# Optimization experiments

Measured on AMD Instinct MI355X. Metric: run time of the kernel, lower is better.

Reference implementation:

```python
import jax, jax.numpy as jnp
import numpy as np

N = 4096
IN_DIM = 128
OUT_DIM = 64
LEAKY_SLOPE = 0.2


def setup_inputs() -> dict:
    key = jax.random.key(0)
    ks = jax.random.split(key, 8)
    H = jax.random.normal(ks[0], (N, IN_DIM), dtype=jnp.float32)
    # dense 0/1 adjacency per relation (int constants w.r.t. autodiff)
    A_buys = jax.random.randint(ks[1], (N, N), 0, 2, dtype=jnp.int32)
    A_views = jax.random.randint(ks[2], (N, N), 0, 2, dtype=jnp.int32)
    # xavier_uniform for W (stored [in, out]; Wh = H @ W == torch Linear with weight W.T)
    s_w = float(np.sqrt(6.0 / (IN_DIM + OUT_DIM)))
    W_buys = jax.random.uniform(ks[3], (IN_DIM, OUT_DIM), jnp.float32, -s_w, s_w)
    W_views = jax.random.uniform(ks[4], (IN_DIM, OUT_DIM), jnp.float32, -s_w, s_w)
    # xavier_uniform on a.view(1, 2*out_dim)
    s_a = float(np.sqrt(6.0 / (1 + 2 * OUT_DIM)))
    a_buys = jax.random.uniform(ks[5], (2 * OUT_DIM,), jnp.float32, -s_a, s_a)
    a_views = jax.random.uniform(ks[6], (2 * OUT_DIM,), jnp.float32, -s_a, s_a)
    bias = jnp.zeros((OUT_DIM,), dtype=jnp.float32)
    return {"H": H, "A_buys": A_buys, "A_views": A_views,
            "W_buys": W_buys, "W_views": W_views,
            "a_buys": a_buys, "a_views": a_views, "bias": bias}


def _relation(H, A, W, a):
    Wh = H @ W                                  # [N, OUT]
    # (cat(Wh_i, Wh_j) * a).sum(-1) == Wh_i @ a[:OUT] + Wh_j @ a[OUT:]
    s_i = Wh @ a[:OUT_DIM]                      # [N]
    s_j = Wh @ a[OUT_DIM:]                      # [N]
    e = jax.nn.leaky_relu(s_i[:, None] + s_j[None, :], LEAKY_SLOPE)  # [N, N]
    e = jnp.where(A == 0, -jnp.inf, e)
    alpha = jnp.nan_to_num(jax.nn.softmax(e, axis=1))                # isolated rows -> 0
    return alpha @ Wh                           # [N, OUT]


def reference(H, A_buys, A_views, W_buys, W_views, a_buys, a_views, bias):
    agg = _relation(H, A_buys, W_buys, a_buys) + _relation(H, A_views, W_views, a_views)
    return agg + bias
```

## Files before the change

### kernel.cpp

```cpp
#include <hip/hip_runtime.h>

#define NN 4096
#define IND 128
#define OUTD 64

typedef __attribute__((ext_vector_type(4))) float  floatx4;
typedef __attribute__((ext_vector_type(8))) __bf16 bf16x8;
typedef __attribute__((ext_vector_type(4))) int    intx4;

__device__ __forceinline__ unsigned short f2bf(float f) {
  unsigned int u = __float_as_uint(f);
  u += 0x7fffu + ((u >> 16) & 1u);
  return (unsigned short)(u >> 16);
}

__device__ __forceinline__ float wcalc(int a, float s) {
  float l = s > 0.f ? s : 0.2f * s;
  float e = __expf(l);
  return a != 0 ? e : 0.f;
}

__global__ __launch_bounds__(256) void gat_prep(
    const float* __restrict__ H,
    const float* __restrict__ W0, const float* __restrict__ W1,
    const float* __restrict__ av0, const float* __restrict__ av1,
    unsigned short* __restrict__ whT,
    float* __restrict__ sA,
    float* __restrict__ sB)
{
  const int rel = blockIdx.y;
  const float* __restrict__ W  = rel ? W1 : W0;
  const float* __restrict__ av = rel ? av1 : av0;
  const int i0 = blockIdx.x * 16;
  const int t = threadIdx.x;
  const int c = t & 63;
  const int wv = __builtin_amdgcn_readfirstlane(t >> 6);
  const float* __restrict__ hp = H + (size_t)(i0 + wv * 4) * IND;

  float acc0 = 0.f, acc1 = 0.f, acc2 = 0.f, acc3 = 0.f;
#pragma unroll 8
  for (int k = 0; k < IND; k += 4) {
    float4 h0 = *(const float4*)(hp + k);
    float4 h1 = *(const float4*)(hp + IND + k);
    float4 h2 = *(const float4*)(hp + 2 * IND + k);
    float4 h3 = *(const float4*)(hp + 3 * IND + k);
    float w0 = W[(k + 0) * OUTD + c];
    float w1 = W[(k + 1) * OUTD + c];
    float w2 = W[(k + 2) * OUTD + c];
    float w3 = W[(k + 3) * OUTD + c];
    acc0 += h0.x * w0 + h0.y * w1 + h0.z * w2 + h0.w * w3;
    acc1 += h1.x * w0 + h1.y * w1 + h1.z * w2 + h1.w * w3;
    acc2 += h2.x * w0 + h2.y * w1 + h2.z * w2 + h2.w * w3;
    acc3 += h3.x * w0 + h3.y * w1 + h3.z * w2 + h3.w * w3;
  }

  const float alo = av[c], ahi = av[OUTD + c];
  float pa0 = acc0 * alo, pa1 = acc1 * alo, pa2 = acc2 * alo, pa3 = acc3 * alo;
  float pb0 = acc0 * ahi, pb1 = acc1 * ahi, pb2 = acc2 * ahi, pb3 = acc3 * ahi;
#pragma unroll
  for (int off = 32; off >= 1; off >>= 1) {
    pa0 += __shfl_xor(pa0, off); pa1 += __shfl_xor(pa1, off);
    pa2 += __shfl_xor(pa2, off); pa3 += __shfl_xor(pa3, off);
    pb0 += __shfl_xor(pb0, off); pb1 += __shfl_xor(pb1, off);
    pb2 += __shfl_xor(pb2, off); pb3 += __shfl_xor(pb3, off);
  }
  const int ibase = i0 + wv * 4;
  if (c == 0) {
    float* sa = sA + rel * NN + ibase;
    float* sb = sB + rel * NN + ibase;
    sa[0] = pa0; sa[1] = pa1; sa[2] = pa2; sa[3] = pa3;
    sb[0] = pb0; sb[1] = pb1; sb[2] = pb2; sb[3] = pb3;
  }

  unsigned long long packed =
      (unsigned long long)f2bf(acc0)        | ((unsigned long long)f2bf(acc1) << 16) |
      ((unsigned long long)f2bf(acc2) << 32) | ((unsigned long long)f2bf(acc3) << 48);
  *(unsigned long long*)(whT + (size_t)(rel * OUTD + c) * NN + ibase) = packed;
}

__global__ __launch_bounds__(512) void gat_main(
    const int* __restrict__ A0, const int* __restrict__ A1,
    const unsigned short* __restrict__ whT,
    const float* __restrict__ sA, const float* __restrict__ sB,
    float* __restrict__ res)
{
  __shared__ float red[8][1024];
  __shared__ float dred[8][16];
  const int rel  = blockIdx.y;
  const int i0   = blockIdx.x * 16;
  const int t    = threadIdx.x;
  const int w    = t >> 6;
  const int lane = t & 63;
  const int m    = lane & 15;
  const int quad = lane >> 4;
  const int i    = i0 + m;
  const int* __restrict__ A = rel ? A1 : A0;
  const float si = sA[rel * NN + i];
  const float* __restrict__ sb = sB + rel * NN;
  const unsigned short* __restrict__ wh = whT + (size_t)rel * OUTD * NN;

  const int jbase = w * 512 + quad * 8;
  const int*            pA  = A  + (size_t)i * NN + jbase;
  const float*          psb = sb + jbase;
  const unsigned short* pb0 = wh + (size_t)(0 * 16 + m) * NN + jbase;
  const unsigned short* pb1 = wh + (size_t)(1 * 16 + m) * NN + jbase;
  const unsigned short* pb2 = wh + (size_t)(2 * 16 + m) * NN + jbase;
  const unsigned short* pb3 = wh + (size_t)(3 * 16 + m) * NN + jbase;

  floatx4 acc0 = {0.f, 0.f, 0.f, 0.f}, acc1 = acc0, acc2 = acc0, acc3 = acc0;
  float dsum = 0.f;

  for (int jt = 0; jt < 512; jt += 32) {
    intx4 a0 = __builtin_nontemporal_load((const intx4*)(pA + jt));
    intx4 a1 = __builtin_nontemporal_load((const intx4*)(pA + jt + 4));
    float4 s0 = *(const float4*)(psb + jt);
    float4 s1 = *(const float4*)(psb + jt + 4);
    bf16x8 b0 = *(const bf16x8*)(pb0 + jt);
    bf16x8 b1 = *(const bf16x8*)(pb1 + jt);
    bf16x8 b2 = *(const bf16x8*)(pb2 + jt);
    bf16x8 b3 = *(const bf16x8*)(pb3 + jt);

    float e0 = wcalc(a0[0], si + s0.x);
    float e1 = wcalc(a0[1], si + s0.y);
    float e2 = wcalc(a0[2], si + s0.z);
    float e3 = wcalc(a0[3], si + s0.w);
    float e4 = wcalc(a1[0], si + s1.x);
    float e5 = wcalc(a1[1], si + s1.y);
    float e6 = wcalc(a1[2], si + s1.z);
    float e7 = wcalc(a1[3], si + s1.w);
    dsum += ((e0 + e1) + (e2 + e3)) + ((e4 + e5) + (e6 + e7));

    bf16x8 af;
    af[0] = (__bf16)e0; af[1] = (__bf16)e1; af[2] = (__bf16)e2; af[3] = (__bf16)e3;
    af[4] = (__bf16)e4; af[5] = (__bf16)e5; af[6] = (__bf16)e6; af[7] = (__bf16)e7;

    acc0 = __builtin_amdgcn_mfma_f32_16x16x32_bf16(af, b0, acc0, 0, 0, 0);
    acc1 = __builtin_amdgcn_mfma_f32_16x16x32_bf16(af, b1, acc1, 0, 0, 0);
    acc2 = __builtin_amdgcn_mfma_f32_16x16x32_bf16(af, b2, acc2, 0, 0, 0);
    acc3 = __builtin_amdgcn_mfma_f32_16x16x32_bf16(af, b3, acc3, 0, 0, 0);
  }

  dsum += __shfl_xor(dsum, 16);
  dsum += __shfl_xor(dsum, 32);

#pragma unroll
  for (int r = 0; r < 4; r++) {
    const int row = quad * 4 + r;
    red[w][row * 64 + 0 * 16 + m] = acc0[r];
    red[w][row * 64 + 1 * 16 + m] = acc1[r];
    red[w][row * 64 + 2 * 16 + m] = acc2[r];
    red[w][row * 64 + 3 * 16 + m] = acc3[r];
  }
  if (lane < 16) dred[w][lane] = dsum;
  __syncthreads();

  const int c  = t & 63;
  const int r0 = t >> 6;
#pragma unroll
  for (int rr = r0; rr < 16; rr += 8) {
    float ns = 0.f, ds = 0.f;
#pragma unroll
    for (int ww = 0; ww < 8; ww++) { ns += red[ww][rr * 64 + c]; ds += dred[ww][rr]; }
    float rv = ds > 0.f ? ns / ds : 0.f;
    res[((size_t)rel * NN + i0 + rr) * OUTD + c] = rv;
  }
}

__global__ __launch_bounds__(256) void gat_combine(
    const float* __restrict__ res, const float* __restrict__ bias,
    float* __restrict__ out)
{
  const int idx = blockIdx.x * 256 + threadIdx.x;
  float4 r0 = ((const float4*)res)[idx];
  float4 r1 = ((const float4*)res)[idx + NN * OUTD / 4];
  float4 b  = ((const float4*)bias)[idx & 15];
  float4 o;
  o.x = r0.x + r1.x + b.x;
  o.y = r0.y + r1.y + b.y;
  o.z = r0.z + r1.z + b.z;
  o.w = r0.w + r1.w + b.w;
  ((float4*)out)[idx] = o;
}

extern "C" void kernel_launch(void* const* d_in, const int* in_sizes, int n_in,
                              void* d_out, int out_size, void* d_ws, size_t ws_size,
                              hipStream_t stream) {
  const float* H    = (const float*)d_in[0];
  const int*   A0   = (const int*)d_in[1];
  const int*   A1   = (const int*)d_in[2];
  const float* W0   = (const float*)d_in[3];
  const float* W1   = (const float*)d_in[4];
  const float* av0  = (const float*)d_in[5];
  const float* av1  = (const float*)d_in[6];
  const float* bias = (const float*)d_in[7];
  float* out = (float*)d_out;

  unsigned short* whT = (unsigned short*)d_ws;
  float* sA  = (float*)((char*)d_ws + 2u * OUTD * NN * 2u);
  float* sB  = sA + 2 * NN;
  float* res = sB + 2 * NN;

  gat_prep<<<dim3(NN / 16, 2), 256, 0, stream>>>(H, W0, W1, av0, av1, whT, sA, sB);
  gat_main<<<dim3(NN / 16, 2), 512, 0, stream>>>(A0, A1, whT, sA, sB, res);
  gat_combine<<<(NN * OUTD / 4) / 256, 256, 0, stream>>>(res, bias, out);
}
```

Baseline: 205.6 us.

## Split attention neighbor dimension across blocks with deferred softmax normalization

The main kernel now splits the j (neighbor) range into two halves across a third grid dimension, doubling the block count. Each block writes unnormalized numerator and denominator partials. The combine kernel sums the partials per relation and divides there. The goal is more parallelism to saturate memory bandwidth on the large adjacency reads, at the cost of extra partial writes and reads. The loop is also unrolled by 2.

```diff
diff --git a/kernel.cpp b/kernel.cpp
--- a/kernel.cpp
+++ b/kernel.cpp
@@ -3,6 +3,7 @@
 #define NN 4096
 #define IND 128
 #define OUTD 64
+#define NSPLIT 2
 
 typedef __attribute__((ext_vector_type(4))) float  floatx4;
 typedef __attribute__((ext_vector_type(8))) __bf16 bf16x8;
@@ -82,11 +83,13 @@
     const int* __restrict__ A0, const int* __restrict__ A1,
     const unsigned short* __restrict__ whT,
     const float* __restrict__ sA, const float* __restrict__ sB,
-    float* __restrict__ res)
+    float* __restrict__ numer,
+    float* __restrict__ denom)
 {
   __shared__ float red[8][1024];
   __shared__ float dred[8][16];
   const int rel  = blockIdx.y;
+  const int sp   = blockIdx.z;
   const int i0   = blockIdx.x * 16;
   const int t    = threadIdx.x;
   const int w    = t >> 6;
@@ -99,7 +102,7 @@
   const float* __restrict__ sb = sB + rel * NN;
   const unsigned short* __restrict__ wh = whT + (size_t)rel * OUTD * NN;
 
-  const int jbase = w * 512 + quad * 8;
+  const int jbase = sp * (NN / NSPLIT) + w * 256 + quad * 8;
   const int*            pA  = A  + (size_t)i * NN + jbase;
   const float*          psb = sb + jbase;
   const unsigned short* pb0 = wh + (size_t)(0 * 16 + m) * NN + jbase;
@@ -110,7 +113,8 @@
   floatx4 acc0 = {0.f, 0.f, 0.f, 0.f}, acc1 = acc0, acc2 = acc0, acc3 = acc0;
   float dsum = 0.f;
 
-  for (int jt = 0; jt < 512; jt += 32) {
+#pragma unroll 2
+  for (int jt = 0; jt < 256; jt += 32) {
     intx4 a0 = __builtin_nontemporal_load((const intx4*)(pA + jt));
     intx4 a1 = __builtin_nontemporal_load((const intx4*)(pA + jt + 4));
     float4 s0 = *(const float4*)(psb + jt);
@@ -156,29 +160,41 @@
 
   const int c  = t & 63;
   const int r0 = t >> 6;
+  const size_t base = ((size_t)rel * NSPLIT + sp) * NN;
 #pragma unroll
   for (int rr = r0; rr < 16; rr += 8) {
     float ns = 0.f, ds = 0.f;
 #pragma unroll
     for (int ww = 0; ww < 8; ww++) { ns += red[ww][rr * 64 + c]; ds += dred[ww][rr]; }
-    float rv = ds > 0.f ? ns / ds : 0.f;
-    res[((size_t)rel * NN + i0 + rr) * OUTD + c] = rv;
+    numer[(base + i0 + rr) * OUTD + c] = ns;
+    if (c == 0) denom[base + i0 + rr] = ds;
   }
 }
 
 __global__ __launch_bounds__(256) void gat_combine(
-    const float* __restrict__ res, const float* __restrict__ bias,
-    float* __restrict__ out)
+    const float* __restrict__ numer, const float* __restrict__ denom,
+    const float* __restrict__ bias, float* __restrict__ out)
 {
   const int idx = blockIdx.x * 256 + threadIdx.x;
-  float4 r0 = ((const float4*)res)[idx];
-  float4 r1 = ((const float4*)res)[idx + NN * OUTD / 4];
-  float4 b  = ((const float4*)bias)[idx & 15];
-  float4 o;
-  o.x = r0.x + r1.x + b.x;
-  o.y = r0.y + r1.y + b.y;
-  o.z = r0.z + r1.z + b.z;
-  o.w = r0.w + r1.w + b.w;
+  const int i  = idx >> 4;
+  const int c4 = idx & 15;
+  const float4* nv = (const float4*)numer;
+
+  float4 o = ((const float4*)bias)[c4];
+#pragma unroll
+  for (int rel = 0; rel < 2; rel++) {
+    float4 n = {0.f, 0.f, 0.f, 0.f};
+    float  d = 0.f;
+#pragma unroll
+    for (int s = 0; s < NSPLIT; s++) {
+      const size_t base = ((size_t)rel * NSPLIT + s) * NN + i;
+      float4 np = nv[base * 16 + c4];
+      n.x += np.x; n.y += np.y; n.z += np.z; n.w += np.w;
+      d += denom[base];
+    }
+    float inv = d > 0.f ? 1.f / d : 0.f;
+    o.x += n.x * inv; o.y += n.y * inv; o.z += n.z * inv; o.w += n.w * inv;
+  }
   ((float4*)out)[idx] = o;
 }
 
@@ -196,11 +212,12 @@
   float* out = (float*)d_out;
 
   unsigned short* whT = (unsigned short*)d_ws;
-  float* sA  = (float*)((char*)d_ws + 2u * OUTD * NN * 2u);
-  float* sB  = sA + 2 * NN;
-  float* res = sB + 2 * NN;
+  float* sA    = (float*)((char*)d_ws + 2u * OUTD * NN * 2u);
+  float* sB    = sA + 2 * NN;
+  float* numer = sB + 2 * NN;
+  float* denom = numer + (size_t)2 * NSPLIT * NN * OUTD;
 
   gat_prep<<<dim3(NN / 16, 2), 256, 0, stream>>>(H, W0, W1, av0, av1, whT, sA, sB);
-  gat_main<<<dim3(NN / 16, 2), 512, 0, stream>>>(A0, A1, whT, sA, sB, res);
-  gat_combine<<<(NN * OUTD / 4) / 256, 256, 0, stream>>>(res, bias, out);
-}
+  gat_main<<<dim3(NN / 16, 2, NSPLIT), 512, 0, stream>>>(A0, A1, whT, sA, sB, numer, denom);
+  gat_combine<<<(NN * OUTD / 4) / 256, 256, 0, stream>>>(numer, denom, bias, out);
+}
```

After: 209.3 us. Within noise of the previous version (+1.8%).
